# Performance work log

Hardware: AMD Instinct MI355X
Metric: run time of the kernel (lower is better)

Reference implementation:

```python
import jax, jax.numpy as jnp
import numpy as np

# paths: per-channel list of (mu, direction) hops; identity path = []
PATHS = [[], [(0, 1)], [(1, 1)], [(2, 1)], [(3, 1)], [(0, -1)], [(1, -1)], [(0, 1), (1, 1)]]
LAT = (32, 32, 32, 32)  # (Lx, Ly, Lz, Lt)


def make_eta(lat):
    """Staggered phases: eta_mu(x) = (-1)**(x_0 + ... + x_{mu-1}); eta_0 = 1.
    Returns float32 array of shape (4, Lx, Ly, Lz, Lt)."""
    coords = jnp.meshgrid(*[jnp.arange(L, dtype=jnp.int32) for L in lat], indexing='ij')
    etas = []
    s = jnp.zeros(lat, dtype=jnp.int32)
    for mu in range(4):
        etas.append(1.0 - 2.0 * (s % 2).astype(jnp.float32))
        s = s + coords[mu]
    return jnp.stack(etas)


def _transport(field, path, U, eta):
    """field: (Lx,Ly,Lz,Lt,3) complex; U: (4,Lx,Ly,Lz,Lt,3,3) complex."""
    for mu, direction in path:
        if direction == 1:
            # eta_mu(x) * U_mu(x) @ field(x + mu_hat)
            shifted = jnp.roll(field, -1, axis=mu)
            t = jnp.einsum('...ab,...b->...a', U[mu], shifted)
            field = eta[mu][..., None].astype(t.dtype) * t
        else:
            # eta_mu(x-mu_hat) * U_mu^dag(x-mu_hat) @ field(x - mu_hat)
            U_dag = jnp.conj(jnp.swapaxes(U[mu], -2, -1))
            U_s = jnp.roll(U_dag, 1, axis=mu)
            f_s = jnp.roll(field, 1, axis=mu)
            t = jnp.einsum('...ab,...b->...a', U_s, f_s)
            field = jnp.roll(eta[mu], 1, axis=mu)[..., None].astype(t.dtype) * t
    return field


def setup_inputs() -> dict:
    key = jax.random.key(0)
    k1, k2, k3, k4 = jax.random.split(key, 4)
    F = len(PATHS)
    x_re = jax.random.normal(k1, (F,) + LAT + (3,), dtype=jnp.float32)
    x_im = jax.random.normal(k2, (F,) + LAT + (3,), dtype=jnp.float32)
    U_re = jax.random.normal(k3, (4,) + LAT + (3, 3), dtype=jnp.float32)
    U_im = jax.random.normal(k4, (4,) + LAT + (3, 3), dtype=jnp.float32)
    return {"x_re": x_re, "x_im": x_im, "U_re": U_re, "U_im": U_im}


def reference(x_re, x_im, U_re, U_im):
    x = jax.lax.complex(x_re, x_im)   # (F, Lx, Ly, Lz, Lt, 3)
    U = jax.lax.complex(U_re, U_im)   # (4, Lx, Ly, Lz, Lt, 3, 3)
    eta = make_eta(LAT)
    out = jnp.stack([_transport(x[i], PATHS[i], U, eta) for i in range(len(PATHS))])
    # return real/imag stacked so the harness sees real float32 output
    return jnp.stack([out.real, out.imag])  # (2, F, Lx, Ly, Lz, Lt, 3)
```

## Files before the change

### kernel.cpp

```cpp
#include <hip/hip_runtime.h>


#define L 32
#define V (32*32*32*32)
#define V3 (V*3)
#define SX (32*32*32)
#define SY (32*32)
#define SZ 32

__device__ __forceinline__ void load_vec(const float* __restrict__ xr,
                                         const float* __restrict__ xi,
                                         int f, int s, float vr[3], float vi[3]) {
    long b = (long)f * V3 + (long)s * 3;
    vr[0] = xr[b+0]; vr[1] = xr[b+1]; vr[2] = xr[b+2];
    vi[0] = xi[b+0]; vi[1] = xi[b+1]; vi[2] = xi[b+2];
}

__device__ __forceinline__ void load_U(const float* __restrict__ Ur_g,
                                       const float* __restrict__ Ui_g,
                                       int mu, int s, float Ur[9], float Ui[9]) {
    long b = (long)mu * (long)V * 9 + (long)s * 9;
#pragma unroll
    for (int k = 0; k < 9; ++k) { Ur[k] = Ur_g[b+k]; Ui[k] = Ui_g[b+k]; }
}

__device__ __forceinline__ void matvec(const float Ur[9], const float Ui[9],
                                       const float vr[3], const float vi[3],
                                       float yr[3], float yi[3]) {
#pragma unroll
    for (int a = 0; a < 3; ++a) {
        float ar = 0.f, ai = 0.f;
#pragma unroll
        for (int b = 0; b < 3; ++b) {
            float ur = Ur[a*3+b], ui = Ui[a*3+b];
            ar += ur * vr[b] - ui * vi[b];
            ai += ur * vi[b] + ui * vr[b];
        }
        yr[a] = ar; yi[a] = ai;
    }
}

__device__ __forceinline__ void matvec_dag(const float Ur[9], const float Ui[9],
                                           const float vr[3], const float vi[3],
                                           float yr[3], float yi[3]) {
#pragma unroll
    for (int a = 0; a < 3; ++a) {
        float ar = 0.f, ai = 0.f;
#pragma unroll
        for (int b = 0; b < 3; ++b) {
            float ur = Ur[b*3+a], ui = Ui[b*3+a];
            ar += ur * vr[b] + ui * vi[b];
            ai += ur * vi[b] - ui * vr[b];
        }
        yr[a] = ar; yi[a] = ai;
    }
}

__device__ __forceinline__ void store_out(float* __restrict__ outr,
                                          float* __restrict__ outi,
                                          int f, int s, float sc,
                                          const float yr[3], const float yi[3]) {
    long b = (long)f * V3 + (long)s * 3;
    outr[b+0] = sc*yr[0]; outr[b+1] = sc*yr[1]; outr[b+2] = sc*yr[2];
    outi[b+0] = sc*yi[0]; outi[b+1] = sc*yi[1]; outi[b+2] = sc*yi[2];
}

__global__ void transport_kernel(const float* __restrict__ xr,
                                 const float* __restrict__ xi,
                                 const float* __restrict__ Urg,
                                 const float* __restrict__ Uig,
                                 float* __restrict__ outr,
                                 float* __restrict__ outi) {
    int s = blockIdx.x * blockDim.x + threadIdx.x;
    if (s >= V) return;

    int t = s & 31;
    int z = (s >> 5) & 31;
    int y = (s >> 10) & 31;
    int x = (s >> 15) & 31;

    int s_xp = s + ((x == 31) ? -(31*SX) : SX);
    int s_xm = s + ((x == 0)  ?  (31*SX) : -SX);
    int s_yp = s + ((y == 31) ? -(31*SY) : SY);
    int s_ym = s + ((y == 0)  ?  (31*SY) : -SY);
    int s_zp = s + ((z == 31) ? -(31*SZ) : SZ);
    int s_tp = s + ((t == 31) ? -31 : 1);
    int s_xpyp = s_yp + ((x == 31) ? -(31*SX) : SX);

    float eta1 = (x & 1) ? -1.f : 1.f;
    float eta2 = ((x + y) & 1) ? -1.f : 1.f;
    float eta3 = ((x + y + z) & 1) ? -1.f : 1.f;

    float vr[3], vi[3], yr[3], yi[3], Ur[9], Ui[9];

    load_vec(xr, xi, 0, s, vr, vi);
    store_out(outr, outi, 0, s, 1.f, vr, vi);

    load_U(Urg, Uig, 0, s, Ur, Ui);
    load_vec(xr, xi, 1, s_xp, vr, vi);
    matvec(Ur, Ui, vr, vi, yr, yi);
    store_out(outr, outi, 1, s, 1.f, yr, yi);

    load_U(Urg, Uig, 1, s, Ur, Ui);
    load_vec(xr, xi, 2, s_yp, vr, vi);
    matvec(Ur, Ui, vr, vi, yr, yi);
    store_out(outr, outi, 2, s, eta1, yr, yi);

    {
        float U1r[9], U1i[9];
#pragma unroll
        for (int k = 0; k < 9; ++k) { U1r[k] = Ur[k]; U1i[k] = Ui[k]; }
        load_U(Urg, Uig, 0, s_yp, Ur, Ui);
        load_vec(xr, xi, 7, s_xpyp, vr, vi);
        float gr[3], gi[3];
        matvec(Ur, Ui, vr, vi, gr, gi);
        matvec(U1r, U1i, gr, gi, yr, yi);
        store_out(outr, outi, 7, s, eta1, yr, yi);
    }

    load_U(Urg, Uig, 2, s, Ur, Ui);
    load_vec(xr, xi, 3, s_zp, vr, vi);
    matvec(Ur, Ui, vr, vi, yr, yi);
    store_out(outr, outi, 3, s, eta2, yr, yi);

    load_U(Urg, Uig, 3, s, Ur, Ui);
    load_vec(xr, xi, 4, s_tp, vr, vi);
    matvec(Ur, Ui, vr, vi, yr, yi);
    store_out(outr, outi, 4, s, eta3, yr, yi);

    load_U(Urg, Uig, 0, s_xm, Ur, Ui);
    load_vec(xr, xi, 5, s_xm, vr, vi);
    matvec_dag(Ur, Ui, vr, vi, yr, yi);
    store_out(outr, outi, 5, s, 1.f, yr, yi);

    load_U(Urg, Uig, 1, s_ym, Ur, Ui);
    load_vec(xr, xi, 6, s_ym, vr, vi);
    matvec_dag(Ur, Ui, vr, vi, yr, yi);
    store_out(outr, outi, 6, s, eta1, yr, yi);
}

extern "C" void kernel_launch(void* const* d_in, const int* in_sizes, int n_in,
                              void* d_out, int out_size, void* d_ws, size_t ws_size,
                              hipStream_t stream) {
    const float* xr  = (const float*)d_in[0];
    const float* xi  = (const float*)d_in[1];
    const float* Urg = (const float*)d_in[2];
    const float* Uig = (const float*)d_in[3];
    float* outr = (float*)d_out;
    float* outi = (float*)d_out + (long)8 * V3;

    const int block = 256;
    const int grid = V / block;
    transport_kernel<<<grid, block, 0, stream>>>(xr, xi, Urg, Uig, outr, outi);
}
```

Baseline: 519.2 us.

## Process four sites per thread with float4 vector loads and nontemporal stores

Each thread now handles four consecutive t-sites, so the 3-vectors and 3x3 link matrices for those sites form contiguous 12- and 36-float chunks that are read with 16-byte vector loads. Outputs are written as float4 nontemporal stores. The t-direction shift is assembled from two neighbouring chunks, and the grid is cut by four. This aims to lower memory-instruction count and improve coalescing, at the cost of much higher register pressure (36-float U arrays per channel), which may lower occupancy or cause spills.

```diff
diff --git a/kernel.cpp b/kernel.cpp
--- a/kernel.cpp
+++ b/kernel.cpp
@@ -1,142 +1,150 @@
 #include <hip/hip_runtime.h>
 
 
-#define L 32
 #define V (32*32*32*32)
 #define V3 (V*3)
 #define SX (32*32*32)
 #define SY (32*32)
 #define SZ 32
 
-__device__ __forceinline__ void load_vec(const float* __restrict__ xr,
-                                         const float* __restrict__ xi,
-                                         int f, int s, float vr[3], float vi[3]) {
-    long b = (long)f * V3 + (long)s * 3;
-    vr[0] = xr[b+0]; vr[1] = xr[b+1]; vr[2] = xr[b+2];
-    vi[0] = xi[b+0]; vi[1] = xi[b+1]; vi[2] = xi[b+2];
+typedef float f4 __attribute__((ext_vector_type(4)));
+
+__device__ __forceinline__ void load12(const float* __restrict__ g, long fidx, float* d) {
+    const f4* q = reinterpret_cast<const f4*>(g + fidx);
+    f4 a = q[0], b = q[1], c = q[2];
+#pragma unroll
+    for (int k = 0; k < 4; ++k) { d[k] = a[k]; d[4+k] = b[k]; d[8+k] = c[k]; }
 }
 
-__device__ __forceinline__ void load_U(const float* __restrict__ Ur_g,
-                                       const float* __restrict__ Ui_g,
-                                       int mu, int s, float Ur[9], float Ui[9]) {
-    long b = (long)mu * (long)V * 9 + (long)s * 9;
+__device__ __forceinline__ void load36(const float* __restrict__ g, long fidx, float* d) {
+    const f4* q = reinterpret_cast<const f4*>(g + fidx);
 #pragma unroll
-    for (int k = 0; k < 9; ++k) { Ur[k] = Ur_g[b+k]; Ui[k] = Ui_g[b+k]; }
-}
-
-__device__ __forceinline__ void matvec(const float Ur[9], const float Ui[9],
-                                       const float vr[3], const float vi[3],
-                                       float yr[3], float yi[3]) {
+    for (int m = 0; m < 9; ++m) {
+        f4 v = q[m];
 #pragma unroll
-    for (int a = 0; a < 3; ++a) {
-        float ar = 0.f, ai = 0.f;
-#pragma unroll
-        for (int b = 0; b < 3; ++b) {
-            float ur = Ur[a*3+b], ui = Ui[a*3+b];
-            ar += ur * vr[b] - ui * vi[b];
-            ai += ur * vi[b] + ui * vr[b];
-        }
-        yr[a] = ar; yi[a] = ai;
+        for (int k = 0; k < 4; ++k) d[4*m + k] = v[k];
     }
 }
 
-__device__ __forceinline__ void matvec_dag(const float Ur[9], const float Ui[9],
-                                           const float vr[3], const float vi[3],
-                                           float yr[3], float yi[3]) {
+__device__ __forceinline__ void store12(float* __restrict__ g, long fidx, const float* d) {
+    f4* q = reinterpret_cast<f4*>(g + fidx);
+    f4 a, b, c;
 #pragma unroll
-    for (int a = 0; a < 3; ++a) {
-        float ar = 0.f, ai = 0.f;
+    for (int k = 0; k < 4; ++k) { a[k] = d[k]; b[k] = d[4+k]; c[k] = d[8+k]; }
+    __builtin_nontemporal_store(a, q + 0);
+    __builtin_nontemporal_store(b, q + 1);
+    __builtin_nontemporal_store(c, q + 2);
+}
+
+template<bool DAG>
+__device__ __forceinline__ void matvec4(const float* Ur, const float* Ui,
+                                        const float* vr, const float* vi,
+                                        float sc, float* yr, float* yi) {
 #pragma unroll
-        for (int b = 0; b < 3; ++b) {
-            float ur = Ur[b*3+a], ui = Ui[b*3+a];
-            ar += ur * vr[b] + ui * vi[b];
-            ai += ur * vi[b] - ui * vr[b];
+    for (int i = 0; i < 4; ++i) {
+#pragma unroll
+        for (int a = 0; a < 3; ++a) {
+            float ar = 0.f, ai = 0.f;
+#pragma unroll
+            for (int b = 0; b < 3; ++b) {
+                float ur = DAG ? Ur[9*i + b*3 + a] : Ur[9*i + a*3 + b];
+                float ui = DAG ? Ui[9*i + b*3 + a] : Ui[9*i + a*3 + b];
+                if (DAG) { ar += ur*vr[3*i+b] + ui*vi[3*i+b];
+                           ai += ur*vi[3*i+b] - ui*vr[3*i+b]; }
+                else     { ar += ur*vr[3*i+b] - ui*vi[3*i+b];
+                           ai += ur*vi[3*i+b] + ui*vr[3*i+b]; }
+            }
+            yr[3*i+a] = sc*ar; yi[3*i+a] = sc*ai;
         }
-        yr[a] = ar; yi[a] = ai;
     }
 }
 
-__device__ __forceinline__ void store_out(float* __restrict__ outr,
-                                          float* __restrict__ outi,
-                                          int f, int s, float sc,
-                                          const float yr[3], const float yi[3]) {
-    long b = (long)f * V3 + (long)s * 3;
-    outr[b+0] = sc*yr[0]; outr[b+1] = sc*yr[1]; outr[b+2] = sc*yr[2];
-    outi[b+0] = sc*yi[0]; outi[b+1] = sc*yi[1]; outi[b+2] = sc*yi[2];
+template<bool DAG>
+__device__ __forceinline__ void channel(const float* __restrict__ xr, const float* __restrict__ xi,
+                                        const float* __restrict__ Urg, const float* __restrict__ Uig,
+                                        float* __restrict__ outr, float* __restrict__ outi,
+                                        int f, int mu, int su, int sv, int s, float sc) {
+    float Ur[36], Ui[36], vr[12], vi[12], yr[12], yi[12];
+    const long ub = (long)mu * V * 9 + (long)su * 9;
+    const long vb = (long)f * V3 + (long)sv * 3;
+    load36(Urg, ub, Ur); load36(Uig, ub, Ui);
+    load12(xr, vb, vr);  load12(xi, vb, vi);
+    matvec4<DAG>(Ur, Ui, vr, vi, sc, yr, yi);
+    const long ob = (long)f * V3 + (long)s * 3;
+    store12(outr, ob, yr); store12(outi, ob, yi);
 }
 
-__global__ void transport_kernel(const float* __restrict__ xr,
-                                 const float* __restrict__ xi,
-                                 const float* __restrict__ Urg,
-                                 const float* __restrict__ Uig,
-                                 float* __restrict__ outr,
-                                 float* __restrict__ outi) {
-    int s = blockIdx.x * blockDim.x + threadIdx.x;
-    if (s >= V) return;
+__global__ __launch_bounds__(256) void transport_kernel(
+        const float* __restrict__ xr, const float* __restrict__ xi,
+        const float* __restrict__ Urg, const float* __restrict__ Uig,
+        float* __restrict__ outr, float* __restrict__ outi) {
+    const int g = blockIdx.x * blockDim.x + threadIdx.x;
+    const int s = g << 2;
+    const int t0 = s & 31;
+    const int z  = (s >> 5)  & 31;
+    const int y  = (s >> 10) & 31;
+    const int x  = (s >> 15) & 31;
 
-    int t = s & 31;
-    int z = (s >> 5) & 31;
-    int y = (s >> 10) & 31;
-    int x = (s >> 15) & 31;
+    const int s_xp   = s + ((x == 31) ? -(31*SX) : SX);
+    const int s_xm   = s + ((x == 0)  ?  (31*SX) : -SX);
+    const int s_yp   = s + ((y == 31) ? -(31*SY) : SY);
+    const int s_ym   = s + ((y == 0)  ?  (31*SY) : -SY);
+    const int s_zp   = s + ((z == 31) ? -(31*SZ) : SZ);
+    const int s_xpyp = s_yp + ((x == 31) ? -(31*SX) : SX);
+    const int s_t1   = (t0 == 28) ? (s - 28) : (s + 4);
 
-    int s_xp = s + ((x == 31) ? -(31*SX) : SX);
-    int s_xm = s + ((x == 0)  ?  (31*SX) : -SX);
-    int s_yp = s + ((y == 31) ? -(31*SY) : SY);
-    int s_ym = s + ((y == 0)  ?  (31*SY) : -SY);
-    int s_zp = s + ((z == 31) ? -(31*SZ) : SZ);
-    int s_tp = s + ((t == 31) ? -31 : 1);
-    int s_xpyp = s_yp + ((x == 31) ? -(31*SX) : SX);
-
-    float eta1 = (x & 1) ? -1.f : 1.f;
-    float eta2 = ((x + y) & 1) ? -1.f : 1.f;
-    float eta3 = ((x + y + z) & 1) ? -1.f : 1.f;
-
-    float vr[3], vi[3], yr[3], yi[3], Ur[9], Ui[9];
-
-    load_vec(xr, xi, 0, s, vr, vi);
-    store_out(outr, outi, 0, s, 1.f, vr, vi);
-
-    load_U(Urg, Uig, 0, s, Ur, Ui);
-    load_vec(xr, xi, 1, s_xp, vr, vi);
-    matvec(Ur, Ui, vr, vi, yr, yi);
-    store_out(outr, outi, 1, s, 1.f, yr, yi);
-
-    load_U(Urg, Uig, 1, s, Ur, Ui);
-    load_vec(xr, xi, 2, s_yp, vr, vi);
-    matvec(Ur, Ui, vr, vi, yr, yi);
-    store_out(outr, outi, 2, s, eta1, yr, yi);
+    const float eta1 = (x & 1) ? -1.f : 1.f;
+    const float eta2 = ((x + y) & 1) ? -1.f : 1.f;
+    const float eta3 = ((x + y + z) & 1) ? -1.f : 1.f;
 
     {
-        float U1r[9], U1i[9];
-#pragma unroll
-        for (int k = 0; k < 9; ++k) { U1r[k] = Ur[k]; U1i[k] = Ui[k]; }
-        load_U(Urg, Uig, 0, s_yp, Ur, Ui);
-        load_vec(xr, xi, 7, s_xpyp, vr, vi);
-        float gr[3], gi[3];
-        matvec(Ur, Ui, vr, vi, gr, gi);
-        matvec(U1r, U1i, gr, gi, yr, yi);
-        store_out(outr, outi, 7, s, eta1, yr, yi);
+        float vr[12], vi[12];
+        const long vb = 0L * V3 + (long)s * 3;
+        load12(xr, vb, vr); load12(xi, vb, vi);
+        store12(outr, vb, vr); store12(outi, vb, vi);
     }
 
-    load_U(Urg, Uig, 2, s, Ur, Ui);
-    load_vec(xr, xi, 3, s_zp, vr, vi);
-    matvec(Ur, Ui, vr, vi, yr, yi);
-    store_out(outr, outi, 3, s, eta2, yr, yi);
+    channel<false>(xr, xi, Urg, Uig, outr, outi, 1, 0, s, s_xp, s, 1.f);
 
-    load_U(Urg, Uig, 3, s, Ur, Ui);
-    load_vec(xr, xi, 4, s_tp, vr, vi);
-    matvec(Ur, Ui, vr, vi, yr, yi);
-    store_out(outr, outi, 4, s, eta3, yr, yi);
+    channel<true >(xr, xi, Urg, Uig, outr, outi, 5, 0, s_xm, s_xm, s, 1.f);
 
-    load_U(Urg, Uig, 0, s_xm, Ur, Ui);
-    load_vec(xr, xi, 5, s_xm, vr, vi);
-    matvec_dag(Ur, Ui, vr, vi, yr, yi);
-    store_out(outr, outi, 5, s, 1.f, yr, yi);
+    channel<false>(xr, xi, Urg, Uig, outr, outi, 2, 1, s, s_yp, s, eta1);
 
-    load_U(Urg, Uig, 1, s_ym, Ur, Ui);
-    load_vec(xr, xi, 6, s_ym, vr, vi);
-    matvec_dag(Ur, Ui, vr, vi, yr, yi);
-    store_out(outr, outi, 6, s, eta1, yr, yi);
+    channel<true >(xr, xi, Urg, Uig, outr, outi, 6, 1, s_ym, s_ym, s, eta1);
+
+    channel<false>(xr, xi, Urg, Uig, outr, outi, 3, 2, s, s_zp, s, eta2);
+
+    {
+        float Ur[36], Ui[36], vr[12], vi[12], yr[12], yi[12];
+        float b0r[12], b0i[12], b1r[12], b1i[12];
+        const long ub  = 3L * (long)V * 9 + (long)s * 9;
+        const long vb0 = 4L * V3 + (long)s * 3;
+        const long vb1 = 4L * V3 + (long)s_t1 * 3;
+        load36(Urg, ub, Ur); load36(Uig, ub, Ui);
+        load12(xr, vb0, b0r); load12(xi, vb0, b0i);
+        load12(xr, vb1, b1r); load12(xi, vb1, b1i);
+#pragma unroll
+        for (int k = 0; k < 9; ++k) { vr[k] = b0r[k+3]; vi[k] = b0i[k+3]; }
+#pragma unroll
+        for (int k = 0; k < 3; ++k) { vr[9+k] = b1r[k]; vi[9+k] = b1i[k]; }
+        matvec4<false>(Ur, Ui, vr, vi, eta3, yr, yi);
+        const long ob = 4L * V3 + (long)s * 3;
+        store12(outr, ob, yr); store12(outi, ob, yi);
+    }
+
+    {
+        float Ur[36], Ui[36], vr[12], vi[12], gr[12], gi[12], yr[12], yi[12];
+        const long ub0 = 0L * (long)V * 9 + (long)s_yp * 9;
+        const long vb  = 7L * V3 + (long)s_xpyp * 3;
+        load36(Urg, ub0, Ur); load36(Uig, ub0, Ui);
+        load12(xr, vb, vr);   load12(xi, vb, vi);
+        matvec4<false>(Ur, Ui, vr, vi, 1.f, gr, gi);
+        const long ub1 = 1L * (long)V * 9 + (long)s * 9;
+        load36(Urg, ub1, Ur); load36(Uig, ub1, Ui);
+        matvec4<false>(Ur, Ui, gr, gi, eta1, yr, yi);
+        const long ob = 7L * V3 + (long)s * 3;
+        store12(outr, ob, yr); store12(outi, ob, yi);
+    }
 }
 
 extern "C" void kernel_launch(void* const* d_in, const int* in_sizes, int n_in,
@@ -150,6 +158,6 @@
     float* outi = (float*)d_out + (long)8 * V3;
 
     const int block = 256;
-    const int grid = V / block;
+    const int grid  = (V / 4) / block;
     transport_kernel<<<grid, block, 0, stream>>>(xr, xi, Urg, Uig, outr, outi);
 }
```

Measured after the change: 653.4 us. 25.9% more time.
